# Kernel tuning notes

Measured on AMD Instinct MI355X. Metric: run time of the kernel, lower is better.

## Reference

```python
import jax, jax.numpy as jnp
import numpy as np

D_MODEL = 256
NUM_HEADS = 8
D_HEAD = D_MODEL // NUM_HEADS  # 32


def setup_inputs() -> dict:
    key = jax.random.key(0)
    ks = jax.random.split(key, 7)
    N, WH = 8, 2048
    s = 1.0 / np.sqrt(D_MODEL)
    return {
        "x": jax.random.normal(ks[0], (N, WH, D_MODEL), dtype=jnp.float32),
        "Wq": jax.random.normal(ks[1], (D_MODEL, D_MODEL), dtype=jnp.float32) * s,
        "bq": jnp.zeros((D_MODEL,), dtype=jnp.float32),
        "Wk": jax.random.normal(ks[2], (D_MODEL, D_MODEL), dtype=jnp.float32) * s,
        "bk": jnp.zeros((D_MODEL,), dtype=jnp.float32),
        "Wv": jax.random.normal(ks[3], (D_MODEL, D_MODEL), dtype=jnp.float32) * s,
        "bv": jnp.zeros((D_MODEL,), dtype=jnp.float32),
    }


def _mhsa(x, Wq, bq, Wk, bk, Wv, bv):
    N, WH, C = x.shape
    # QKV projections; reshape to (N, heads, WH, d_head)
    def split_heads(t):
        return t.reshape(N, WH, NUM_HEADS, D_HEAD).transpose(0, 2, 1, 3)
    Q = split_heads(x @ Wq + bq)
    K = split_heads(x @ Wk + bk)
    V = split_heads(x @ Wv + bv)
    # FAITHFUL to source: logits /= d_k**(-0.5)  ==  logits * sqrt(d_k)
    logits = jnp.einsum("nhqd,nhkd->nhqk", Q, K) * jnp.sqrt(jnp.float32(D_HEAD))
    attn = jax.nn.softmax(logits, axis=-1)  # dropout p=0.1 is identity in eval
    x_attn = jnp.einsum("nhqk,nhkd->nhqd", attn, V)
    x_attn = x_attn.transpose(0, 2, 1, 3).reshape(N, WH, C)
    # drop_path is identity in eval mode; residual add
    return x_attn + x


def reference(x, Wq, bq, Wk, bk, Wv, bv):
    return _mhsa(x, Wq, bq, Wk, bk, Wv, bv)
```

## Files before the change

kernel.cpp:

```cpp
#include <hip/hip_runtime.h>
#include <math.h>

#define WH 2048
#define DM 256
#define NHD 8
#define DH 32
#define NB 8

typedef __attribute__((ext_vector_type(8))) short short8;
typedef __attribute__((ext_vector_type(4))) short short4v;
typedef __attribute__((ext_vector_type(4))) float f32x4;

__device__ __forceinline__ unsigned short bf16_rn(float f) {
    unsigned u = __float_as_uint(f);
    return (unsigned short)((u + 0x8000u) >> 16);
}
__device__ __forceinline__ float bf16_to_f(unsigned short h) {
    return __uint_as_float(((unsigned)h) << 16);
}
__device__ __forceinline__ unsigned pack_bf16_rn(float f1, float f0) {
    return __builtin_amdgcn_perm(__float_as_uint(f1) + 0x8000u,
                                 __float_as_uint(f0) + 0x8000u, 0x07060302);
}
__device__ __forceinline__ void glds16(const void* g, void* l) {
    __builtin_amdgcn_global_load_lds(
        (const __attribute__((address_space(1))) unsigned int*)g,
        (__attribute__((address_space(3))) unsigned int*)l, 16, 0, 0);
}

__global__ __launch_bounds__(256) void xprep(
    const float* __restrict__ X,
    unsigned short* __restrict__ Xhi, unsigned short* __restrict__ Xlo)
{
    const size_t i = ((size_t)blockIdx.x * 256 + threadIdx.x) * 8;
    const int row = (int)(i >> 8);
    const int k   = (int)(i & 255);
    const size_t dst = ((size_t)(k >> 5) * 16384 + row) * 32 + (k & 31);
    float4 a = *(const float4*)&X[i];
    float4 b = *(const float4*)&X[i + 4];
    float v[8] = {a.x, a.y, a.z, a.w, b.x, b.y, b.z, b.w};
    short8 hi, lo;
    #pragma unroll
    for (int e = 0; e < 8; e++) {
        unsigned short hb = bf16_rn(v[e]);
        hi[e] = (short)hb;
        lo[e] = (short)bf16_rn(v[e] - bf16_to_f(hb));
    }
    *(short8*)&Xhi[dst] = hi;
    *(short8*)&Xlo[dst] = lo;
}

__global__ __launch_bounds__(256) void wprep(
    const float* __restrict__ Wq, const float* __restrict__ Wk,
    const float* __restrict__ Wv,
    unsigned short* __restrict__ WThi, unsigned short* __restrict__ WTlo)
{
    const int z = blockIdx.y;
    const float* W = (z == 0) ? Wq : ((z == 1) ? Wk : Wv);
    const size_t zoff = (size_t)z * DM * DM;
    const int tg = blockIdx.x * 256 + threadIdx.x;
    #pragma unroll
    for (int j = 0; j < 4; j++) {
        const int f = tg + j * 4096;
        const int k  = f >> 6;
        const int n0 = (f & 63) * 4;
        float4 v = *(const float4*)&W[(size_t)k * DM + n0];
        float vv[4] = {v.x, v.y, v.z, v.w};
        #pragma unroll
        for (int i = 0; i < 4; i++) {
            unsigned short hb = bf16_rn(vv[i]);
            const size_t dst = zoff + ((size_t)(k >> 5) * 256 + n0 + i) * 32 + (k & 31);
            WThi[dst] = hb;
            WTlo[dst] = bf16_rn(vv[i] - bf16_to_f(hb));
        }
    }
}

__global__ __launch_bounds__(256, 1) void qkv_mfma(
    const unsigned short* __restrict__ Xhi, const unsigned short* __restrict__ Xlo,
    const unsigned short* __restrict__ WThi, const unsigned short* __restrict__ WTlo,
    const float* __restrict__ bq, const float* __restrict__ bk, const float* __restrict__ bv,
    unsigned short* __restrict__ Qhi, unsigned short* __restrict__ Qlo,
    unsigned short* __restrict__ KV)
{
    __shared__ __align__(16) unsigned short arena[4 * 2 * 4096];

    const int z = blockIdx.z;
    const float* bias = (z == 0) ? bq : ((z == 1) ? bk : bv);
    const size_t zoff = (size_t)z * DM * DM;

    const int tid  = threadIdx.x;
    const int w    = tid >> 6;
    const int lane = tid & 63;
    const int col  = lane & 15;
    const int quad = lane >> 4;
    const int wr = w >> 1, wc = w & 1;
    const int bm = blockIdx.x * 128;
    const int bn = blockIdx.y * 128;

    const int perm16 = (((lane & 3) ^ ((lane >> 3) & 3))) * 16;
    const char* glane; size_t kstr;
    if (w == 0)      { glane = (const char*)Xhi + (size_t)(bm + (lane >> 2)) * 64 + perm16; kstr = (size_t)16384 * 64; }
    else if (w == 1) { glane = (const char*)Xlo + (size_t)(bm + (lane >> 2)) * 64 + perm16; kstr = (size_t)16384 * 64; }
    else if (w == 2) { glane = (const char*)(WThi + zoff) + (size_t)(bn + (lane >> 2)) * 64 + perm16; kstr = 256 * 64; }
    else             { glane = (const char*)(WTlo + zoff) + (size_t)(bn + (lane >> 2)) * 64 + perm16; kstr = 256 * 64; }

    auto issue = [&](int kb, int b) {
        const char* g0 = glane + (size_t)kb * kstr;
        unsigned short* l0 = &arena[w * 8192 + b * 4096];
        #pragma unroll
        for (int g = 0; g < 8; g++)
            glds16(g0 + (size_t)g * 1024, l0 + g * 512);
    };

    f32x4 acc[4][4];
    #pragma unroll
    for (int mi = 0; mi < 4; mi++)
        #pragma unroll
        for (int ni = 0; ni < 4; ni++) acc[mi][ni] = (f32x4){0.f, 0.f, 0.f, 0.f};

    const int sw = (col >> 1) & 3;
    const int fO = (quad ^ sw) * 8;

    issue(0, 0);
    __syncthreads();
    for (int kb = 0; kb < 8; kb++) {
        const int b = kb & 1;
        if (kb < 7) issue(kb + 1, b ^ 1);

        short8 ah[4], al[4], bh[4], bl[4];
        #pragma unroll
        for (int mi = 0; mi < 4; mi++) {
            const int ro = (wr * 64 + mi * 16 + col) * 32 + fO;
            ah[mi] = *(const short8*)&arena[        b * 4096 + ro];
            al[mi] = *(const short8*)&arena[ 8192 + b * 4096 + ro];
        }
        #pragma unroll
        for (int ni = 0; ni < 4; ni++) {
            const int no = (wc * 64 + ni * 16 + col) * 32 + fO;
            bh[ni] = *(const short8*)&arena[16384 + b * 4096 + no];
            bl[ni] = *(const short8*)&arena[24576 + b * 4096 + no];
        }
        #pragma unroll
        for (int mi = 0; mi < 4; mi++)
            #pragma unroll
            for (int ni = 0; ni < 4; ni++) {
                acc[mi][ni] = __builtin_amdgcn_mfma_f32_16x16x32_bf16(al[mi], bh[ni], acc[mi][ni], 0, 0, 0);
                acc[mi][ni] = __builtin_amdgcn_mfma_f32_16x16x32_bf16(ah[mi], bl[ni], acc[mi][ni], 0, 0, 0);
                acc[mi][ni] = __builtin_amdgcn_mfma_f32_16x16x32_bf16(ah[mi], bh[ni], acc[mi][ni], 0, 0, 0);
            }
        __syncthreads();
    }

    unsigned* Tp = (unsigned*)arena;
    const int n   = bm >> 11;
    const int wqb = bm & (WH - 1);
    const float qsc = (z == 0) ? 8.1611159f : 1.0f;

    #pragma unroll
    for (int p = 0; p < 2; p++) {
        if (wr == p) {
            #pragma unroll
            for (int mi = 0; mi < 4; mi++)
                #pragma unroll
                for (int ni = 0; ni < 4; ni++) {
                    const int lc = wc * 64 + ni * 16 + col;
                    const float bb = bias[bn + lc];
                    #pragma unroll
                    for (int r = 0; r < 4; r++) {
                        float v = (acc[mi][ni][r] + bb) * qsc;
                        unsigned short hb = bf16_rn(v);
                        unsigned short lb = bf16_rn(v - bf16_to_f(hb));
                        Tp[(mi * 16 + quad * 4 + r) * 132 + lc] =
                            (unsigned)hb | ((unsigned)lb << 16);
                    }
                }
        }
        __syncthreads();
        if (z == 2) {
            const int c = tid >> 1, half = tid & 1;
            const int coln = bn + c, h = coln >> 5, d = coln & 31;
            const int key0 = wqb + p * 64 + half * 32;
            const int t = key0 >> 6, k6 = key0 & 63;
            unsigned short* dst =
                &KV[(((size_t)(n * NHD + h) * 32 + t) * 6144) + 4096 + d * 64 + k6];
            unsigned hi[16];
            #pragma unroll
            for (int jj = 0; jj < 16; jj++) {
                unsigned u0 = Tp[(half * 32 + 2 * jj    ) * 132 + c];
                unsigned u1 = Tp[(half * 32 + 2 * jj + 1) * 132 + c];
                hi[jj] = __builtin_amdgcn_perm(u1, u0, 0x05040100);
            }
            #pragma unroll
            for (int s = 0; s < 4; s++)
                *(uint4*)&dst[s * 8] = make_uint4(hi[4*s], hi[4*s+1], hi[4*s+2], hi[4*s+3]);
        } else if (z == 1) {
            const int lr = tid >> 2, seg = tid & 3;
            const int h = (bn + seg * 32) >> 5;
            const int key = wqb + p * 64 + lr;
            const int t = key >> 6, k6 = key & 63;
            unsigned short* blobK =
                &KV[(((size_t)(n * NHD + h) * 32 + t) * 6144) + k6 * 32];
            #pragma unroll
            for (int s = 0; s < 4; s++) {
                unsigned u[8], hi[4], lo[4];
                *(uint4*)&u[0] = *(uint4*)&Tp[lr * 132 + seg * 32 + s * 8];
                *(uint4*)&u[4] = *(uint4*)&Tp[lr * 132 + seg * 32 + s * 8 + 4];
                #pragma unroll
                for (int jj = 0; jj < 4; jj++) {
                    hi[jj] = __builtin_amdgcn_perm(u[2*jj+1], u[2*jj], 0x05040100);
                    lo[jj] = __builtin_amdgcn_perm(u[2*jj+1], u[2*jj], 0x07060302);
                }
                *(uint4*)&blobK[s * 8]        = make_uint4(hi[0], hi[1], hi[2], hi[3]);
                *(uint4*)&blobK[2048 + s * 8] = make_uint4(lo[0], lo[1], lo[2], lo[3]);
            }
        } else {
            const int lr = tid >> 2, seg = tid & 3;
            const int h = (bn + seg * 32) >> 5;
            const size_t off = ((size_t)((n * NHD + h) * WH) + wqb + p * 64 + lr) * DH;
            #pragma unroll
            for (int s = 0; s < 4; s++) {
                unsigned u[8], hi[4], lo[4];
                *(uint4*)&u[0] = *(uint4*)&Tp[lr * 132 + seg * 32 + s * 8];
                *(uint4*)&u[4] = *(uint4*)&Tp[lr * 132 + seg * 32 + s * 8 + 4];
                #pragma unroll
                for (int jj = 0; jj < 4; jj++) {
                    hi[jj] = __builtin_amdgcn_perm(u[2*jj+1], u[2*jj], 0x05040100);
                    lo[jj] = __builtin_amdgcn_perm(u[2*jj+1], u[2*jj], 0x07060302);
                }
                *(uint4*)&Qhi[off + s * 8] = make_uint4(hi[0], hi[1], hi[2], hi[3]);
                *(uint4*)&Qlo[off + s * 8] = make_uint4(lo[0], lo[1], lo[2], lo[3]);
            }
        }
        __syncthreads();
    }
}

__global__ __launch_bounds__(256, 4) void attn(
    const unsigned short* __restrict__ Qhi, const unsigned short* __restrict__ Qlo,
    const unsigned short* __restrict__ KV,  const float* __restrict__ X,
    float* __restrict__ Out)
{
    __shared__ __align__(16) unsigned short B[2][6144];

    const int tid  = threadIdx.x;
    const int w    = tid >> 6;
    const int lane = tid & 63;
    const int col  = lane & 15;
    const int quad = lane >> 4;
    const int nh   = blockIdx.y;
    const int q0   = blockIdx.x * 128;
    const size_t qbase = (size_t)nh * WH * DH;
    const char* blob = (const char*)(KV + (size_t)nh * 196608);

    short8 qh[2], ql[2];
    #pragma unroll
    for (int f = 0; f < 2; f++) {
        const int qrow = q0 + f * 64 + w * 16 + col;
        qh[f] = *(const short8*)&Qhi[qbase + (size_t)qrow * DH + quad * 8];
        ql[f] = *(const short8*)&Qlo[qbase + (size_t)qrow * DH + quad * 8];
    }

    f32x4 o00 = {0.f,0.f,0.f,0.f}, o01 = {0.f,0.f,0.f,0.f};
    f32x4 o10 = {0.f,0.f,0.f,0.f}, o11 = {0.f,0.f,0.f,0.f};
    float mr0 = -INFINITY, mr1 = -INFINITY, lr0 = 0.f, lr1 = 0.f;

    const char* gseg[3];
    int loseg[3];
    #pragma unroll
    for (int j = 0; j < 3; j++) {
        const int s = w * 3 + j;
        int loff;
        if (s < 8) loff = (lane >> 2) * 64  + (((lane & 3) ^ ((lane >> 3) & 3)) << 4);
        else       loff = (lane >> 3) * 128 + (((lane & 7) ^ ((lane >> 3) & 7)) << 4);
        gseg[j] = blob + s * 1024 + loff;
        loseg[j] = s * 512;
    }

    auto issue = [&](int t, int b) {
        #pragma unroll
        for (int j = 0; j < 3; j++)
            glds16(gseg[j] + (size_t)t * 12288, &B[b][loseg[j]]);
    };

    const int sw = (col >> 1) & 3;

    auto body = [&](int b) {
        const unsigned short* Bp = &B[b][0];
        short8 kh[4], kl[4];
        #pragma unroll
        for (int kc = 0; kc < 4; kc++) {
            const int ro = (col + kc * 16) * 32 + (quad ^ sw) * 8;
            kh[kc] = *(const short8*)&Bp[ro];
            kl[kc] = *(const short8*)&Bp[2048 + ro];
        }
        short4v va[4][2];
        #pragma unroll
        for (int kc = 0; kc < 4; kc++) {
            const int cl = kc * 2 + (quad >> 1);
            const int co = ((cl ^ (col & 7)) << 3) + (quad & 1) * 4;
            va[kc][0] = *(const short4v*)&Bp[4096 + (col     ) * 64 + co];
            va[kc][1] = *(const short4v*)&Bp[4096 + (col + 16) * 64 + co];
        }
        #pragma unroll
        for (int f = 0; f < 2; f++) {
            f32x4 s[4];
            #pragma unroll
            for (int kc = 0; kc < 4; kc++) {
                f32x4 a = {0.f, 0.f, 0.f, 0.f};
                a = __builtin_amdgcn_mfma_f32_16x16x32_bf16(kh[kc], ql[f], a, 0, 0, 0);
                a = __builtin_amdgcn_mfma_f32_16x16x32_bf16(kl[kc], qh[f], a, 0, 0, 0);
                a = __builtin_amdgcn_mfma_f32_16x16x32_bf16(kh[kc], qh[f], a, 0, 0, 0);
                s[kc] = a;
            }
            float mx = s[0][0];
            #pragma unroll
            for (int kc = 0; kc < 4; kc++)
                #pragma unroll
                for (int r = 0; r < 4; r++) mx = fmaxf(mx, s[kc][r]);
            mx = fmaxf(mx, __shfl_xor(mx, 16));
            mx = fmaxf(mx, __shfl_xor(mx, 32));
            float& mrf = f ? mr1 : mr0;
            float& lrf = f ? lr1 : lr0;
            const float mnew  = fmaxf(mrf, mx);
            const float alpha = __builtin_amdgcn_exp2f(mrf - mnew);

            float ps = 0.f;
            #pragma unroll
            for (int kc = 0; kc < 4; kc++)
                #pragma unroll
                for (int r = 0; r < 4; r++) {
                    s[kc][r] = __builtin_amdgcn_exp2f(s[kc][r] - mnew);
                    ps += s[kc][r];
                }
            lrf = lrf * alpha + ps;
            mrf = mnew;

            short4v pb[4];
            #pragma unroll
            for (int kc = 0; kc < 4; kc++) {
                union { short4v v; unsigned u[2]; } P;
                P.u[0] = pack_bf16_rn(s[kc][1], s[kc][0]);
                P.u[1] = pack_bf16_rn(s[kc][3], s[kc][2]);
                pb[kc] = P.v;
            }

            f32x4& a0 = f ? o10 : o00;
            f32x4& a1 = f ? o11 : o01;
            #pragma unroll
            for (int r = 0; r < 4; r++) { a0[r] *= alpha; a1[r] *= alpha; }
            #pragma unroll
            for (int kc = 0; kc < 4; kc++) {
                a0 = __builtin_amdgcn_mfma_f32_16x16x16bf16_1k(va[kc][0], pb[kc], a0, 0, 0, 0);
                a1 = __builtin_amdgcn_mfma_f32_16x16x16bf16_1k(va[kc][1], pb[kc], a1, 0, 0, 0);
            }
        }
    };

    issue(0, 0);
    __syncthreads();
    for (int t2 = 0; t2 < 16; t2++) {
        issue(2 * t2 + 1, 1);
        body(0);
        __syncthreads();
        if (t2 < 15) issue(2 * t2 + 2, 0);
        body(1);
        __syncthreads();
    }

    const int n = nh >> 3, h = nh & 7;
    #pragma unroll
    for (int f = 0; f < 2; f++) {
        float l = f ? lr1 : lr0;
        l += __shfl_xor(l, 16);
        l += __shfl_xor(l, 32);
        const float inv = 1.f / l;
        const f32x4& a0 = f ? o10 : o00;
        const f32x4& a1 = f ? o11 : o01;
        const int qrow = q0 + f * 64 + w * 16 + col;
        const size_t a = ((size_t)n * WH + qrow) * DM + h * DH + quad * 4;
        float4 x0 = *(const float4*)&X[a];
        float4 y0;
        y0.x = a0[0] * inv + x0.x;
        y0.y = a0[1] * inv + x0.y;
        y0.z = a0[2] * inv + x0.z;
        y0.w = a0[3] * inv + x0.w;
        *(float4*)&Out[a] = y0;
        float4 x1 = *(const float4*)&X[a + 16];
        float4 y1;
        y1.x = a1[0] * inv + x1.x;
        y1.y = a1[1] * inv + x1.y;
        y1.z = a1[2] * inv + x1.z;
        y1.w = a1[3] * inv + x1.w;
        *(float4*)&Out[a + 16] = y1;
    }
}

extern "C" void kernel_launch(void* const* d_in, const int* in_sizes, int n_in,
                              void* d_out, int out_size, void* d_ws, size_t ws_size,
                              hipStream_t stream) {
    const float* x  = (const float*)d_in[0];
    const float* Wq = (const float*)d_in[1];
    const float* bq = (const float*)d_in[2];
    const float* Wk = (const float*)d_in[3];
    const float* bk = (const float*)d_in[4];
    const float* Wv = (const float*)d_in[5];
    const float* bv = (const float*)d_in[6];
    float* out = (float*)d_out;

    const size_t elems = (size_t)NB * WH * DM;
    unsigned short* Qhi  = (unsigned short*)d_ws;
    unsigned short* Qlo  = Qhi + elems;
    unsigned short* KV   = Qlo + elems;
    unsigned short* WThi = KV  + (size_t)64 * 32 * 6144;
    unsigned short* WTlo = WThi + (size_t)3 * DM * DM;

    unsigned short* Xhi = (unsigned short*)d_out;
    unsigned short* Xlo = Xhi + elems;

    xprep<<<2048, 256, 0, stream>>>(x, Xhi, Xlo);

    dim3 gw(16, 3);
    wprep<<<gw, 256, 0, stream>>>(Wq, Wk, Wv, WThi, WTlo);

    dim3 gg(128, 2, 3);
    qkv_mfma<<<gg, 256, 0, stream>>>(Xhi, Xlo, WThi, WTlo, bq, bk, bv,
                                     Qhi, Qlo, KV);

    dim3 ga(WH / 128, NB * NHD);
    attn<<<ga, 256, 0, stream>>>(Qhi, Qlo, KV, x, out);
}
```

Before: 217.8 us.

## Merge prep kernels, single-buffer QKV GEMM, lazy softmax rescale with MFMA row sums

```diff
diff --git a/kernel.cpp b/kernel.cpp
--- a/kernel.cpp
+++ b/kernel.cpp
@@ -18,9 +18,8 @@
 __device__ __forceinline__ float bf16_to_f(unsigned short h) {
     return __uint_as_float(((unsigned)h) << 16);
 }
-__device__ __forceinline__ unsigned pack_bf16_rn(float f1, float f0) {
-    return __builtin_amdgcn_perm(__float_as_uint(f1) + 0x8000u,
-                                 __float_as_uint(f0) + 0x8000u, 0x07060302);
+__device__ __forceinline__ unsigned pack_bf16_rtz(float f1, float f0) {
+    return __builtin_amdgcn_perm(__float_as_uint(f1), __float_as_uint(f0), 0x07060302);
 }
 __device__ __forceinline__ void glds16(const void* g, void* l) {
     __builtin_amdgcn_global_load_lds(
@@ -28,62 +27,62 @@
         (__attribute__((address_space(3))) unsigned int*)l, 16, 0, 0);
 }
 
-__global__ __launch_bounds__(256) void xprep(
+__global__ __launch_bounds__(256) void prep(
     const float* __restrict__ X,
-    unsigned short* __restrict__ Xhi, unsigned short* __restrict__ Xlo)
-{
-    const size_t i = ((size_t)blockIdx.x * 256 + threadIdx.x) * 8;
-    const int row = (int)(i >> 8);
-    const int k   = (int)(i & 255);
-    const size_t dst = ((size_t)(k >> 5) * 16384 + row) * 32 + (k & 31);
-    float4 a = *(const float4*)&X[i];
-    float4 b = *(const float4*)&X[i + 4];
-    float v[8] = {a.x, a.y, a.z, a.w, b.x, b.y, b.z, b.w};
-    short8 hi, lo;
-    #pragma unroll
-    for (int e = 0; e < 8; e++) {
-        unsigned short hb = bf16_rn(v[e]);
-        hi[e] = (short)hb;
-        lo[e] = (short)bf16_rn(v[e] - bf16_to_f(hb));
-    }
-    *(short8*)&Xhi[dst] = hi;
-    *(short8*)&Xlo[dst] = lo;
-}
-
-__global__ __launch_bounds__(256) void wprep(
-    const float* __restrict__ Wq, const float* __restrict__ Wk,
-    const float* __restrict__ Wv,
+    const float* __restrict__ Wq, const float* __restrict__ Wk, const float* __restrict__ Wv,
+    unsigned short* __restrict__ Xhi, unsigned short* __restrict__ Xlo,
     unsigned short* __restrict__ WThi, unsigned short* __restrict__ WTlo)
 {
-    const int z = blockIdx.y;
-    const float* W = (z == 0) ? Wq : ((z == 1) ? Wk : Wv);
-    const size_t zoff = (size_t)z * DM * DM;
-    const int tg = blockIdx.x * 256 + threadIdx.x;
-    #pragma unroll
-    for (int j = 0; j < 4; j++) {
-        const int f = tg + j * 4096;
-        const int k  = f >> 6;
-        const int n0 = (f & 63) * 4;
-        float4 v = *(const float4*)&W[(size_t)k * DM + n0];
-        float vv[4] = {v.x, v.y, v.z, v.w};
-        #pragma unroll
-        for (int i = 0; i < 4; i++) {
-            unsigned short hb = bf16_rn(vv[i]);
-            const size_t dst = zoff + ((size_t)(k >> 5) * 256 + n0 + i) * 32 + (k & 31);
-            WThi[dst] = hb;
-            WTlo[dst] = bf16_rn(vv[i] - bf16_to_f(hb));
-        }
-    }
-}
-
-__global__ __launch_bounds__(256, 1) void qkv_mfma(
+    const int bid = blockIdx.x;
+    if (bid < 2048) {
+        const size_t i = ((size_t)bid * 256 + threadIdx.x) * 8;
+        const int row = (int)(i >> 8);
+        const int k   = (int)(i & 255);
+        const size_t dst = ((size_t)(k >> 5) * 16384 + row) * 32 + (k & 31);
+        float4 a = *(const float4*)&X[i];
+        float4 b = *(const float4*)&X[i + 4];
+        float v[8] = {a.x, a.y, a.z, a.w, b.x, b.y, b.z, b.w};
+        short8 hi, lo;
+        #pragma unroll
+        for (int e = 0; e < 8; e++) {
+            unsigned short hb = bf16_rn(v[e]);
+            hi[e] = (short)hb;
+            lo[e] = (short)bf16_rn(v[e] - bf16_to_f(hb));
+        }
+        *(short8*)&Xhi[dst] = hi;
+        *(short8*)&Xlo[dst] = lo;
+    } else {
+        const int b2 = bid - 2048;
+        const int z = b2 >> 4, xb = b2 & 15;
+        const float* W = (z == 0) ? Wq : ((z == 1) ? Wk : Wv);
+        const size_t zoff = (size_t)z * DM * DM;
+        const int tg = xb * 256 + threadIdx.x;
+        #pragma unroll
+        for (int j = 0; j < 4; j++) {
+            const int f = tg + j * 4096;
+            const int k  = f >> 6;
+            const int n0 = (f & 63) * 4;
+            float4 v = *(const float4*)&W[(size_t)k * DM + n0];
+            float vv[4] = {v.x, v.y, v.z, v.w};
+            #pragma unroll
+            for (int i = 0; i < 4; i++) {
+                unsigned short hb = bf16_rn(vv[i]);
+                const size_t dst = zoff + ((size_t)(k >> 5) * 256 + n0 + i) * 32 + (k & 31);
+                WThi[dst] = hb;
+                WTlo[dst] = bf16_rn(vv[i] - bf16_to_f(hb));
+            }
+        }
+    }
+}
+
+__global__ __launch_bounds__(256, 3) void qkv_mfma(
     const unsigned short* __restrict__ Xhi, const unsigned short* __restrict__ Xlo,
     const unsigned short* __restrict__ WThi, const unsigned short* __restrict__ WTlo,
     const float* __restrict__ bq, const float* __restrict__ bk, const float* __restrict__ bv,
     unsigned short* __restrict__ Qhi, unsigned short* __restrict__ Qlo,
     unsigned short* __restrict__ KV)
 {
-    __shared__ __align__(16) unsigned short arena[4 * 2 * 4096];
+    __shared__ __align__(16) unsigned short arena[16896];
 
     const int z = blockIdx.z;
     const float* bias = (z == 0) ? bq : ((z == 1) ? bk : bv);
@@ -105,9 +104,9 @@
     else if (w == 2) { glane = (const char*)(WThi + zoff) + (size_t)(bn + (lane >> 2)) * 64 + perm16; kstr = 256 * 64; }
     else             { glane = (const char*)(WTlo + zoff) + (size_t)(bn + (lane >> 2)) * 64 + perm16; kstr = 256 * 64; }
 
-    auto issue = [&](int kb, int b) {
+    auto issue = [&](int kb) {
         const char* g0 = glane + (size_t)kb * kstr;
-        unsigned short* l0 = &arena[w * 8192 + b * 4096];
+        unsigned short* l0 = &arena[w * 4096];
         #pragma unroll
         for (int g = 0; g < 8; g++)
             glds16(g0 + (size_t)g * 1024, l0 + g * 512);
@@ -122,24 +121,22 @@
     const int sw = (col >> 1) & 3;
     const int fO = (quad ^ sw) * 8;
 
-    issue(0, 0);
-    __syncthreads();
     for (int kb = 0; kb < 8; kb++) {
-        const int b = kb & 1;
-        if (kb < 7) issue(kb + 1, b ^ 1);
+        issue(kb);
+        __syncthreads();
 
         short8 ah[4], al[4], bh[4], bl[4];
         #pragma unroll
         for (int mi = 0; mi < 4; mi++) {
             const int ro = (wr * 64 + mi * 16 + col) * 32 + fO;
-            ah[mi] = *(const short8*)&arena[        b * 4096 + ro];
-            al[mi] = *(const short8*)&arena[ 8192 + b * 4096 + ro];
+            ah[mi] = *(const short8*)&arena[ro];
+            al[mi] = *(const short8*)&arena[4096 + ro];
         }
         #pragma unroll
         for (int ni = 0; ni < 4; ni++) {
             const int no = (wc * 64 + ni * 16 + col) * 32 + fO;
-            bh[ni] = *(const short8*)&arena[16384 + b * 4096 + no];
-            bl[ni] = *(const short8*)&arena[24576 + b * 4096 + no];
+            bh[ni] = *(const short8*)&arena[8192 + no];
+            bl[ni] = *(const short8*)&arena[12288 + no];
         }
         #pragma unroll
         for (int mi = 0; mi < 4; mi++)
@@ -263,7 +260,8 @@
 
     f32x4 o00 = {0.f,0.f,0.f,0.f}, o01 = {0.f,0.f,0.f,0.f};
     f32x4 o10 = {0.f,0.f,0.f,0.f}, o11 = {0.f,0.f,0.f,0.f};
-    float mr0 = -INFINITY, mr1 = -INFINITY, lr0 = 0.f, lr1 = 0.f;
+    f32x4 la0 = {0.f,0.f,0.f,0.f}, la1 = {0.f,0.f,0.f,0.f};
+    float mr0 = 0.f, mr1 = 0.f;
 
     const char* gseg[3];
     int loseg[3];
@@ -284,6 +282,7 @@
     };
 
     const int sw = (col >> 1) & 3;
+    const short4v ones = {(short)0x3F80, (short)0x3F80, (short)0x3F80, (short)0x3F80};
 
     auto body = [&](int b) {
         const unsigned short* Bp = &B[b][0];
@@ -320,39 +319,37 @@
                 for (int r = 0; r < 4; r++) mx = fmaxf(mx, s[kc][r]);
             mx = fmaxf(mx, __shfl_xor(mx, 16));
             mx = fmaxf(mx, __shfl_xor(mx, 32));
+
             float& mrf = f ? mr1 : mr0;
-            float& lrf = f ? lr1 : lr0;
-            const float mnew  = fmaxf(mrf, mx);
-            const float alpha = __builtin_amdgcn_exp2f(mrf - mnew);
-
-            float ps = 0.f;
-            #pragma unroll
-            for (int kc = 0; kc < 4; kc++)
-                #pragma unroll
-                for (int r = 0; r < 4; r++) {
-                    s[kc][r] = __builtin_amdgcn_exp2f(s[kc][r] - mnew);
-                    ps += s[kc][r];
-                }
-            lrf = lrf * alpha + ps;
-            mrf = mnew;
-
-            short4v pb[4];
-            #pragma unroll
-            for (int kc = 0; kc < 4; kc++) {
-                union { short4v v; unsigned u[2]; } P;
-                P.u[0] = pack_bf16_rn(s[kc][1], s[kc][0]);
-                P.u[1] = pack_bf16_rn(s[kc][3], s[kc][2]);
-                pb[kc] = P.v;
-            }
-
             f32x4& a0 = f ? o10 : o00;
             f32x4& a1 = f ? o11 : o01;
-            #pragma unroll
-            for (int r = 0; r < 4; r++) { a0[r] *= alpha; a1[r] *= alpha; }
+            f32x4& la = f ? la1 : la0;
+            const float mnew = fmaxf(mrf, mx);
+            if (__any(mx > mrf)) {
+                const float alpha = __builtin_amdgcn_exp2f(mrf - mnew);
+                #pragma unroll
+                for (int r = 0; r < 4; r++) { a0[r] *= alpha; a1[r] *= alpha; }
+                la[0] *= alpha;
+            }
+            mrf = mnew;
+
+            short4v pb[4];
+            #pragma unroll
+            for (int kc = 0; kc < 4; kc++) {
+                const float p0 = __builtin_amdgcn_exp2f(s[kc][0] - mnew);
+                const float p1 = __builtin_amdgcn_exp2f(s[kc][1] - mnew);
+                const float p2 = __builtin_amdgcn_exp2f(s[kc][2] - mnew);
+                const float p3 = __builtin_amdgcn_exp2f(s[kc][3] - mnew);
+                union { short4v v; unsigned u[2]; } P;
+                P.u[0] = pack_bf16_rtz(p1, p0);
+                P.u[1] = pack_bf16_rtz(p3, p2);
+                pb[kc] = P.v;
+            }
             #pragma unroll
             for (int kc = 0; kc < 4; kc++) {
                 a0 = __builtin_amdgcn_mfma_f32_16x16x16bf16_1k(va[kc][0], pb[kc], a0, 0, 0, 0);
                 a1 = __builtin_amdgcn_mfma_f32_16x16x16bf16_1k(va[kc][1], pb[kc], a1, 0, 0, 0);
+                la = __builtin_amdgcn_mfma_f32_16x16x16bf16_1k(ones,      pb[kc], la, 0, 0, 0);
             }
         }
     };
@@ -371,10 +368,7 @@
     const int n = nh >> 3, h = nh & 7;
     #pragma unroll
     for (int f = 0; f < 2; f++) {
-        float l = f ? lr1 : lr0;
-        l += __shfl_xor(l, 16);
-        l += __shfl_xor(l, 32);
-        const float inv = 1.f / l;
+        const float inv = 1.f / (f ? la1[0] : la0[0]);
         const f32x4& a0 = f ? o10 : o00;
         const f32x4& a1 = f ? o11 : o01;
         const int qrow = q0 + f * 64 + w * 16 + col;
@@ -418,10 +412,7 @@
     unsigned short* Xhi = (unsigned short*)d_out;
     unsigned short* Xlo = Xhi + elems;
 
-    xprep<<<2048, 256, 0, stream>>>(x, Xhi, Xlo);
-
-    dim3 gw(16, 3);
-    wprep<<<gw, 256, 0, stream>>>(Wq, Wk, Wv, WThi, WTlo);
+    prep<<<2096, 256, 0, stream>>>(x, Wq, Wk, Wv, Xhi, Xlo, WThi, WTlo);
 
     dim3 gg(128, 2, 3);
     qkv_mfma<<<gg, 256, 0, stream>>>(Xhi, Xlo, WThi, WTlo, bq, bk, bv,
```

Result: faster. 205.0 us, median of 2 (-5.9%).
